# Kernel tuning notes

Measured on AMD Instinct MI355X. Metric: run time of the kernel, lower is better.

Reference implementation:

```python
import jax, jax.numpy as jnp
import numpy as np

B, T, C, H = 8, 1024, 768, 12  # GPT-2 small attention, block_size=1024

def setup_inputs() -> dict:
    key = jax.random.key(0)
    k0, k1, k2 = jax.random.split(key, 3)
    return {
        "x": jax.random.normal(k0, (1, B, T, C), jnp.float32) * 0.02,
        "w_attn": jax.random.normal(k1, (C, 3 * C), jnp.float32) * 0.02,
        "b_attn": jnp.zeros((3 * C,), jnp.float32),
        "w_proj": jax.random.normal(k2, (C, C), jnp.float32) * 0.02,
        "b_proj": jnp.zeros((C,), jnp.float32),
    }

def reference(x, w_attn, b_attn, w_proj, b_proj):
    _, b, t, c = x.shape
    d = c // H  # head dim
    xb = x[0]  # [B,T,C]
    qkv = xb @ w_attn + b_attn  # [B,T,3C]
    q, k, v = jnp.split(qkv, 3, axis=-1)
    def to_heads(u):
        return u.reshape(b, t, H, d).transpose(0, 2, 1, 3)  # [B,H,T,D]
    q, k, v = to_heads(q), to_heads(k), to_heads(v)
    scale = 1.0 / jnp.sqrt(jnp.asarray(d, q.dtype))
    att = jnp.einsum('bhqd,bhkd->bhqk', q, k) * scale  # [B,H,T,T]
    causal = jnp.tril(jnp.ones((t, t), bool))
    att = jnp.where(causal, att, -jnp.inf)
    att = jax.nn.softmax(att, axis=-1)
    y = jnp.einsum('bhqk,bhkd->bhqd', att, v)  # [B,H,T,D]
    y = y.transpose(0, 2, 1, 3).reshape(1, b, t, c)
    return y @ w_proj + b_proj
```

## Files before the change

kernel.cpp:

```cpp
#include <hip/hip_runtime.h>
#include <hip/hip_bf16.h>
#include <math.h>

#define Bq 8
#define Tq 1024
#define Cq 768
#define Hq 12
#define Dq 64
#define MROWS (Bq*Tq)
#define N_QKV (3*Cq)

typedef __bf16 bf16;
typedef bf16 bf16x8 __attribute__((ext_vector_type(8)));
typedef bf16 bf16x4 __attribute__((ext_vector_type(4)));
typedef float f32x4 __attribute__((ext_vector_type(4)));
typedef float f32x16 __attribute__((ext_vector_type(16)));
typedef unsigned int u32x4 __attribute__((ext_vector_type(4)));

#define MFMA16x16x32(a, b, c) __builtin_amdgcn_mfma_f32_16x16x32_bf16((a), (b), (c), 0, 0, 0)
#define MFMA32x32x16(a, b, c) __builtin_amdgcn_mfma_f32_32x32x16_bf16((a), (b), (c), 0, 0, 0)

__device__ __forceinline__ bf16x8& lds_v8(bf16* base, int row, int byteoff) {
    return *reinterpret_cast<bf16x8*>(
        reinterpret_cast<char*>(base) + row * 128 + (byteoff ^ ((row & 7) << 4)));
}

typedef __attribute__((address_space(3))) unsigned int lds_u32;
typedef const __attribute__((address_space(1))) unsigned int glb_u32;
__device__ __forceinline__ void gload16(const void* g, void* lds) {
    __builtin_amdgcn_global_load_lds((glb_u32*)(uintptr_t)g,
                                     (lds_u32*)(unsigned int)(uintptr_t)lds,
                                     16, 0, 0);
}

__device__ __forceinline__ unsigned cvtpk_bf16(float lo, float hi) {
    unsigned r;
    asm volatile("v_cvt_pk_bf16_f32 %0, %1, %2" : "=v"(r) : "v"(lo), "v"(hi));
    return r;
}

#define NA_CONV 3072
#define NB_WA   432
#define NB_WP   144
__global__ __launch_bounds__(256) void prep(const float* __restrict__ x,
                                            const float* __restrict__ wa,
                                            const float* __restrict__ wp,
                                            bf16* __restrict__ Ax,
                                            bf16* __restrict__ WaT,
                                            bf16* __restrict__ WpT) {
    __shared__ float tile[64][65];
    const int bid = blockIdx.x;
    if (bid < NA_CONV) {
        const int i = bid * 256 + threadIdx.x;
        const float4* p = reinterpret_cast<const float4*>(x) + (size_t)i * 2;
        float4 a = p[0], b = p[1];
        bf16x8 o;
        o[0] = (bf16)a.x; o[1] = (bf16)a.y; o[2] = (bf16)a.z; o[3] = (bf16)a.w;
        o[4] = (bf16)b.x; o[5] = (bf16)b.y; o[6] = (bf16)b.z; o[7] = (bf16)b.w;
        reinterpret_cast<bf16x8*>(Ax)[i] = o;
        return;
    }
    const float* src;
    bf16* dst;
    int C, tb, bxT;
    if (bid < NA_CONV + NB_WA) { tb = bid - NA_CONV; src = wa; dst = WaT; C = N_QKV; bxT = 36; }
    else                       { tb = bid - NA_CONV - NB_WA; src = wp; dst = WpT; C = Cq; bxT = 12; }
    const int R = Cq;
    const int bx = (tb % bxT) * 64, by = (tb / bxT) * 64;
    const int tx = threadIdx.x & 63, ty = threadIdx.x >> 6;
    #pragma unroll
    for (int i = 0; i < 64; i += 4)
        tile[ty + i][tx] = src[(size_t)(by + ty + i) * C + bx + tx];
    __syncthreads();
    #pragma unroll
    for (int i = 0; i < 64; i += 4)
        dst[(size_t)(bx + ty + i) * R + by + tx] = (bf16)tile[tx][ty + i];
}

__global__ __launch_bounds__(256) void gemm_qkv(const bf16* __restrict__ A,
                                                const bf16* __restrict__ Bt,
                                                const float* __restrict__ bias,
                                                bf16* __restrict__ Qo,
                                                bf16* __restrict__ Ko,
                                                bf16* __restrict__ Vto) {
    __shared__ bf16 As[2][128 * 64];
    __shared__ bf16 Bs[2][128 * 64];
    const int tid = threadIdx.x;
    const int w = tid >> 6, l = tid & 63;
    const int lane16 = l & 15, kg = l >> 4;
    const int wr = w >> 1, wc = w & 1;
    const int flat = blockIdx.x;
    const int nid = (flat & 7) * 144 + (flat >> 3);
    const int bn0 = (nid % 18) * 128, bm0 = (nid / 18) * 128;

    auto stage = [&](int k0, int buf) {
        #pragma unroll
        for (int j = 0; j < 4; ++j) {
            const int q8 = w * 4 + j;
            const int r  = q8 * 8 + (l >> 3);
            const int c16 = (l & 7) ^ (r & 7);
            gload16(A + (size_t)(bm0 + r) * Cq + k0 + c16 * 8, &As[buf][q8 * 512]);
            gload16(Bt + (size_t)(bn0 + r) * Cq + k0 + c16 * 8, &Bs[buf][q8 * 512]);
        }
    };

    f32x4 acc[4][4] = {};
    stage(0, 0);
    __syncthreads();
    for (int kt = 0; kt < 12; ++kt) {
        if (kt < 11) stage((kt + 1) * 64, (kt + 1) & 1);
        bf16* Ac = As[kt & 1];
        bf16* Bc = Bs[kt & 1];
        #pragma unroll
        for (int ks = 0; ks < 2; ++ks) {
            bf16x8 af[4], bfr[4];
            #pragma unroll
            for (int m = 0; m < 4; ++m)
                af[m] = lds_v8(Ac, wr * 64 + m * 16 + lane16, ks * 64 + kg * 16);
            #pragma unroll
            for (int n = 0; n < 4; ++n)
                bfr[n] = lds_v8(Bc, wc * 64 + n * 16 + lane16, ks * 64 + kg * 16);
            #pragma unroll
            for (int m = 0; m < 4; ++m)
                #pragma unroll
                for (int n = 0; n < 4; ++n)
                    acc[m][n] = MFMA16x16x32(af[m], bfr[n], acc[m][n]);
        }
        __syncthreads();
    }

    const int whichB = bn0 / Cq;
    char* Lt = (char*)&As[0][0];
    #pragma unroll
    for (int mi = 0; mi < 4; ++mi) {
        #pragma unroll
        for (int r = 0; r < 4; ++r) {
            const int m = wr * 64 + mi * 16 + kg * 4 + r;
            #pragma unroll
            for (int ni = 0; ni < 4; ++ni) {
                const int n = wc * 64 + ni * 16 + lane16;
                float v = acc[mi][ni][r] + bias[bn0 + n];
                if (whichB == 0) v *= 0.18033688011112042f;
                int a;
                if (whichB < 2) a = m * 256 + ((n * 2) ^ ((m & 7) << 4));
                else            a = n * 256 + ((m * 2) ^ ((n & 7) << 4));
                *reinterpret_cast<bf16*>(Lt + a) = (bf16)v;
            }
        }
    }
    __syncthreads();
    const int bb = bm0 >> 10, tt0 = bm0 & 1023;
    if (whichB < 2) {
        bf16* dst = whichB == 0 ? Qo : Ko;
        #pragma unroll
        for (int j = 0; j < 8; ++j) {
            const int c = j * 256 + tid;
            const int m = c >> 4, nc = c & 15;
            bf16x8 val = *reinterpret_cast<bf16x8*>(Lt + m * 256 + ((nc * 16) ^ ((m & 7) << 4)));
            const int gcol0 = bn0 + nc * 8;
            const int h = (gcol0 - whichB * Cq) >> 6;
            const int d0 = gcol0 & 63;
            *reinterpret_cast<bf16x8*>(dst + (((size_t)bb * Hq + h) * Tq + tt0 + m) * Dq + d0) = val;
        }
    } else {
        #pragma unroll
        for (int j = 0; j < 8; ++j) {
            const int c = j * 256 + tid;
            const int n = c >> 4, mc = c & 15;
            bf16x8 val = *reinterpret_cast<bf16x8*>(Lt + n * 256 + ((mc * 16) ^ ((n & 7) << 4)));
            const int gcol0 = bn0 + n;
            const int h = (gcol0 - 2 * Cq) >> 6;
            const int d = gcol0 & 63;
            *reinterpret_cast<bf16x8*>(Vto + (((size_t)bb * Hq + h) * Dq + d) * Tq + tt0 + mc * 8) = val;
        }
    }
}

__global__ __launch_bounds__(256) void attn_mfma(const bf16* __restrict__ Q,
                                                 const bf16* __restrict__ K,
                                                 const bf16* __restrict__ Vt,
                                                 bf16* __restrict__ Y) {
    const int tid = threadIdx.x;
    const int w = tid >> 6, l = tid & 63;
    const int l31 = l & 31, hi = l >> 5;
    const int g = blockIdx.x / 96;
    const int bh = blockIdx.x % 96;
    const int qs = 31 - (g * 4 + w);
    const int q0 = qs * 32;
    const int nt = (qs >> 1) + 1;
    const size_t hoff = (size_t)bh * Tq * Dq;

    bf16x8 qf[4];
    #pragma unroll
    for (int ds = 0; ds < 4; ++ds)
        qf[ds] = *reinterpret_cast<const bf16x8*>(
            Q + hoff + (size_t)(q0 + l31) * Dq + ds * 16 + hi * 8);

    f32x16 o[2] = {};
    float m_ = -INFINITY, l_ = 0.f;

    for (int t = 0; t < nt; ++t) {
        const bool diag = (t == nt - 1);
        const bool half = diag && !(qs & 1);
        const bf16* Kt  = K  + hoff + (size_t)(t * 64) * Dq;
        const bf16* Vtt = Vt + hoff + t * 64;

        bf16x8 kf0[4], kf1[4];
        #pragma unroll
        for (int ds = 0; ds < 4; ++ds)
            kf0[ds] = *reinterpret_cast<const bf16x8*>(
                Kt + (size_t)l31 * Dq + ds * 16 + hi * 8);
        if (!half) {
            #pragma unroll
            for (int ds = 0; ds < 4; ++ds)
                kf1[ds] = *reinterpret_cast<const bf16x8*>(
                    Kt + (size_t)(32 + l31) * Dq + ds * 16 + hi * 8);
        }
        bf16x8 vf[4][2];
        #pragma unroll
        for (int ks = 0; ks < 2; ++ks)
            #pragma unroll
            for (int dh = 0; dh < 2; ++dh)
                vf[ks][dh] = *reinterpret_cast<const bf16x8*>(
                    Vtt + (size_t)(dh * 32 + l31) * Tq + ks * 16 + hi * 8);
        if (!half) {
            #pragma unroll
            for (int ks = 2; ks < 4; ++ks)
                #pragma unroll
                for (int dh = 0; dh < 2; ++dh)
                    vf[ks][dh] = *reinterpret_cast<const bf16x8*>(
                        Vtt + (size_t)(dh * 32 + l31) * Tq + ks * 16 + hi * 8);
        }

        f32x16 s0 = {}, s1 = {};
        #pragma unroll
        for (int ds = 0; ds < 4; ++ds) s0 = MFMA32x32x16(kf0[ds], qf[ds], s0);
        if (!half) {
            #pragma unroll
            for (int ds = 0; ds < 4; ++ds) s1 = MFMA32x32x16(kf1[ds], qf[ds], s1);
        }
        if (diag) {
            #pragma unroll
            for (int reg = 0; reg < 16; ++reg) {
                const int kg_ = t * 64 + (reg & 3) + 8 * (reg >> 2) + 4 * hi;
                if (kg_ > q0 + l31) s0[reg] = -INFINITY;
                if (!half && kg_ + 32 > q0 + l31) s1[reg] = -INFINITY;
            }
        }
        float pmax = -INFINITY;
        #pragma unroll
        for (int reg = 0; reg < 16; ++reg) pmax = fmaxf(pmax, s0[reg]);
        if (!half) {
            #pragma unroll
            for (int reg = 0; reg < 16; ++reg) pmax = fmaxf(pmax, s1[reg]);
        }
        pmax = fmaxf(pmax, __shfl_xor(pmax, 32));
        if (!__all(pmax <= m_ + 8.f)) {
            const float mn = fmaxf(m_, pmax);
            const float alpha = exp2f(m_ - mn);
            m_ = mn;
            l_ *= alpha;
            o[0] *= alpha;
            o[1] *= alpha;
        }
        float lsum = 0.f;
        #pragma unroll
        for (int reg = 0; reg < 16; ++reg) {
            const float p = exp2f(s0[reg] - m_);
            s0[reg] = p;
            lsum += p;
        }
        if (!half) {
            #pragma unroll
            for (int reg = 0; reg < 16; ++reg) {
                const float p = exp2f(s1[reg] - m_);
                s1[reg] = p;
                lsum += p;
            }
        }
        l_ += lsum;

        bf16x8 pa[4];
        #pragma unroll
        for (int g2 = 0; g2 < 2; ++g2) {
            const int rb = g2 * 8;
            const unsigned u01 = cvtpk_bf16(s0[rb + 0], s0[rb + 1]);
            const unsigned u23 = cvtpk_bf16(s0[rb + 2], s0[rb + 3]);
            const unsigned u45 = cvtpk_bf16(s0[rb + 4], s0[rb + 5]);
            const unsigned u67 = cvtpk_bf16(s0[rb + 6], s0[rb + 7]);
            const unsigned x01 = __shfl_xor(u01, 32);
            const unsigned x23 = __shfl_xor(u23, 32);
            const unsigned x45 = __shfl_xor(u45, 32);
            const unsigned x67 = __shfl_xor(u67, 32);
            u32x4 wv;
            wv[0] = hi ? x45 : u01;
            wv[1] = hi ? x67 : u23;
            wv[2] = hi ? u45 : x01;
            wv[3] = hi ? u67 : x23;
            pa[g2] = __builtin_bit_cast(bf16x8, wv);
        }
        if (!half) {
            #pragma unroll
            for (int g2 = 0; g2 < 2; ++g2) {
                const int rb = g2 * 8;
                const unsigned u01 = cvtpk_bf16(s1[rb + 0], s1[rb + 1]);
                const unsigned u23 = cvtpk_bf16(s1[rb + 2], s1[rb + 3]);
                const unsigned u45 = cvtpk_bf16(s1[rb + 4], s1[rb + 5]);
                const unsigned u67 = cvtpk_bf16(s1[rb + 6], s1[rb + 7]);
                const unsigned x01 = __shfl_xor(u01, 32);
                const unsigned x23 = __shfl_xor(u23, 32);
                const unsigned x45 = __shfl_xor(u45, 32);
                const unsigned x67 = __shfl_xor(u67, 32);
                u32x4 wv;
                wv[0] = hi ? x45 : u01;
                wv[1] = hi ? x67 : u23;
                wv[2] = hi ? u45 : x01;
                wv[3] = hi ? u67 : x23;
                pa[2 + g2] = __builtin_bit_cast(bf16x8, wv);
            }
        }
        #pragma unroll
        for (int ks = 0; ks < 2; ++ks)
            #pragma unroll
            for (int dh = 0; dh < 2; ++dh)
                o[dh] = MFMA32x32x16(vf[ks][dh], pa[ks], o[dh]);
        if (!half) {
            #pragma unroll
            for (int ks = 2; ks < 4; ++ks)
                #pragma unroll
                for (int dh = 0; dh < 2; ++dh)
                    o[dh] = MFMA32x32x16(vf[ks][dh], pa[ks], o[dh]);
        }
    }

    const int bb = bh / Hq, h = bh - bb * Hq;
    const float ltot = l_ + __shfl_xor(l_, 32);
    const float inv = 1.f / ltot;
    bf16* yp = Y + ((size_t)bb * Tq + q0 + l31) * Cq + h * Dq;
    #pragma unroll
    for (int dh = 0; dh < 2; ++dh)
        #pragma unroll
        for (int rg = 0; rg < 4; ++rg) {
            const int d0 = 8 * rg + 4 * hi + 32 * dh;
            bf16x4 ov;
            #pragma unroll
            for (int j = 0; j < 4; ++j) ov[j] = (bf16)(o[dh][rg * 4 + j] * inv);
            *reinterpret_cast<bf16x4*>(yp + d0) = ov;
        }
}

__global__ __launch_bounds__(256) void gemm_proj(const bf16* __restrict__ A,
                                                 const bf16* __restrict__ Bt,
                                                 const float* __restrict__ bias,
                                                 float* __restrict__ out) {
    __shared__ bf16 As[2][128 * 64];
    __shared__ bf16 Bs[2][128 * 64];
    const int tid = threadIdx.x;
    const int w = tid >> 6, l = tid & 63;
    const int lane16 = l & 15, kg = l >> 4;
    const int wr = w >> 1, wc = w & 1;
    const int flat = blockIdx.x;
    const int nid = (flat & 7) * 48 + (flat >> 3);
    const int bn0 = (nid % 6) * 128, bm0 = (nid / 6) * 128;

    auto stage = [&](int k0, int buf) {
        #pragma unroll
        for (int j = 0; j < 4; ++j) {
            const int q8 = w * 4 + j;
            const int r  = q8 * 8 + (l >> 3);
            const int c16 = (l & 7) ^ (r & 7);
            gload16(A + (size_t)(bm0 + r) * Cq + k0 + c16 * 8, &As[buf][q8 * 512]);
            gload16(Bt + (size_t)(bn0 + r) * Cq + k0 + c16 * 8, &Bs[buf][q8 * 512]);
        }
    };

    f32x4 acc[4][4] = {};
    stage(0, 0);
    __syncthreads();
    for (int kt = 0; kt < 12; ++kt) {
        if (kt < 11) stage((kt + 1) * 64, (kt + 1) & 1);
        bf16* Ac = As[kt & 1];
        bf16* Bc = Bs[kt & 1];
        #pragma unroll
        for (int ks = 0; ks < 2; ++ks) {
            bf16x8 af[4], bfr[4];
            #pragma unroll
            for (int m = 0; m < 4; ++m)
                af[m] = lds_v8(Ac, wr * 64 + m * 16 + lane16, ks * 64 + kg * 16);
            #pragma unroll
            for (int n = 0; n < 4; ++n)
                bfr[n] = lds_v8(Bc, wc * 64 + n * 16 + lane16, ks * 64 + kg * 16);
            #pragma unroll
            for (int m = 0; m < 4; ++m)
                #pragma unroll
                for (int n = 0; n < 4; ++n)
                    acc[m][n] = MFMA16x16x32(af[m], bfr[n], acc[m][n]);
        }
        __syncthreads();
    }

    char* L32 = (char*)&As[0][0];
    #pragma unroll
    for (int half = 0; half < 2; ++half) {
        if (wc == half) {
            #pragma unroll
            for (int mi = 0; mi < 4; ++mi)
                #pragma unroll
                for (int r = 0; r < 4; ++r) {
                    const int m = wr * 64 + mi * 16 + kg * 4 + r;
                    #pragma unroll
                    for (int ni = 0; ni < 4; ++ni) {
                        const int nl = ni * 16 + lane16;
                        const float v = acc[mi][ni][r] + bias[bn0 + half * 64 + nl];
                        *reinterpret_cast<float*>(L32 + m * 256 + ((nl * 4) ^ ((m & 7) << 4))) = v;
                    }
                }
        }
        __syncthreads();
        #pragma unroll
        for (int j = 0; j < 8; ++j) {
            const int c = j * 256 + tid;
            const int m = c >> 4, nc = c & 15;
            float4 val = *reinterpret_cast<float4*>(L32 + m * 256 + ((nc * 16) ^ ((m & 7) << 4)));
            *reinterpret_cast<float4*>(out + (size_t)(bm0 + m) * Cq + bn0 + half * 64 + nc * 4) = val;
        }
        __syncthreads();
    }
}

extern "C" void kernel_launch(void* const* d_in, const int* in_sizes, int n_in,
                              void* d_out, int out_size, void* d_ws, size_t ws_size,
                              hipStream_t stream) {
    const float* x      = (const float*)d_in[0];
    const float* w_attn = (const float*)d_in[1];
    const float* b_attn = (const float*)d_in[2];
    const float* w_proj = (const float*)d_in[3];
    const float* b_proj = (const float*)d_in[4];
    float* out = (float*)d_out;

    char* ws = (char*)d_ws;
    bf16* Ax  = (bf16*)ws; ws += (size_t)MROWS * Cq * 2;
    bf16* WaT = (bf16*)ws; ws += (size_t)N_QKV * Cq * 2;
    bf16* WpT = (bf16*)ws; ws += (size_t)Cq * Cq * 2;
    bf16* Qw  = (bf16*)ws; ws += (size_t)MROWS * Cq * 2;
    bf16* Kw  = (bf16*)ws; ws += (size_t)MROWS * Cq * 2;
    bf16* Vtw = (bf16*)ws; ws += (size_t)MROWS * Cq * 2;
    bf16* Yw  = (bf16*)ws; ws += (size_t)MROWS * Cq * 2;

    prep<<<dim3(NA_CONV + NB_WA + NB_WP), 256, 0, stream>>>(x, w_attn, w_proj, Ax, WaT, WpT);
    gemm_qkv<<<dim3(1152), 256, 0, stream>>>(Ax, WaT, b_attn, Qw, Kw, Vtw);
    attn_mfma<<<dim3(768), 256, 0, stream>>>(Qw, Kw, Vtw, Yw);
    gemm_proj<<<dim3(384), 256, 0, stream>>>(Yw, WpT, b_proj, out);
}
```

Before: 125.0 us.

## Stage K/V tiles in double-buffered LDS shared across waves in attention

The attention kernel now loads each 64-key K and V^T tile once per block into a double-buffered, swizzled LDS buffer using async global-to-LDS loads, prefetching the next tile while computing the current one. Before, each wave read K/V directly from global memory. The block-to-(head, query-block) mapping is also rearranged so the four waves share a head and adjacent query slices, with XCD-aware ordering. This cuts redundant global traffic and overlaps loads with compute, but adds a __syncthreads per tile and makes waves with shorter causal ranges wait for the longest one.

```diff
diff --git a/kernel.cpp b/kernel.cpp
--- a/kernel.cpp
+++ b/kernel.cpp
@@ -180,14 +180,19 @@
                                                  const bf16* __restrict__ K,
                                                  const bf16* __restrict__ Vt,
                                                  bf16* __restrict__ Y) {
+    __shared__ bf16 Kl[2][64 * 64];
+    __shared__ bf16 Vl[2][64 * 64];
     const int tid = threadIdx.x;
     const int w = tid >> 6, l = tid & 63;
     const int l31 = l & 31, hi = l >> 5;
-    const int g = blockIdx.x / 96;
-    const int bh = blockIdx.x % 96;
-    const int qs = 31 - (g * 4 + w);
+    const int id = blockIdx.x;
+    const int xcd = id & 7, j = id >> 3;
+    const int bh = xcd * 12 + (j >> 3);
+    const int qb = 7 - (j & 7);
+    const int qs = qb * 4 + w;
     const int q0 = qs * 32;
     const int nt = (qs >> 1) + 1;
+    const int ntmax = 2 * qb + 2;
     const size_t hoff = (size_t)bh * Tq * Dq;
 
     bf16x8 qf[4];
@@ -199,114 +204,94 @@
     f32x16 o[2] = {};
     float m_ = -INFINITY, l_ = 0.f;
 
-    for (int t = 0; t < nt; ++t) {
-        const bool diag = (t == nt - 1);
-        const bool half = diag && !(qs & 1);
-        const bf16* Kt  = K  + hoff + (size_t)(t * 64) * Dq;
-        const bf16* Vtt = Vt + hoff + t * 64;
-
-        bf16x8 kf0[4], kf1[4];
-        #pragma unroll
-        for (int ds = 0; ds < 4; ++ds)
-            kf0[ds] = *reinterpret_cast<const bf16x8*>(
-                Kt + (size_t)l31 * Dq + ds * 16 + hi * 8);
-        if (!half) {
+    auto stage = [&](int t, int buf) {
+        #pragma unroll
+        for (int jj = 0; jj < 2; ++jj) {
+            const int q8 = w * 2 + jj;
+            const int r  = q8 * 8 + (l >> 3);
+            const int c16 = (l & 7) ^ (r & 7);
+            gload16(K + hoff + (size_t)(t * 64 + r) * Dq + c16 * 8, &Kl[buf][q8 * 512]);
+            gload16(Vt + hoff + (size_t)r * Tq + t * 64 + c16 * 8, &Vl[buf][q8 * 512]);
+        }
+    };
+
+    stage(0, 0);
+    __syncthreads();
+
+    for (int t = 0; t < ntmax; ++t) {
+        if (t + 1 < ntmax) stage(t + 1, (t + 1) & 1);
+        if (t < nt) {
+            bf16* Kc = Kl[t & 1];
+            bf16* Vc = Vl[t & 1];
+            const bool diag = (t == nt - 1);
+            const bool half = diag && !(qs & 1);
+
+            bf16x8 kf0[4], kf1[4];
             #pragma unroll
             for (int ds = 0; ds < 4; ++ds)
-                kf1[ds] = *reinterpret_cast<const bf16x8*>(
-                    Kt + (size_t)(32 + l31) * Dq + ds * 16 + hi * 8);
-        }
-        bf16x8 vf[4][2];
-        #pragma unroll
-        for (int ks = 0; ks < 2; ++ks)
-            #pragma unroll
-            for (int dh = 0; dh < 2; ++dh)
-                vf[ks][dh] = *reinterpret_cast<const bf16x8*>(
-                    Vtt + (size_t)(dh * 32 + l31) * Tq + ks * 16 + hi * 8);
-        if (!half) {
-            #pragma unroll
-            for (int ks = 2; ks < 4; ++ks)
-                #pragma unroll
-                for (int dh = 0; dh < 2; ++dh)
-                    vf[ks][dh] = *reinterpret_cast<const bf16x8*>(
-                        Vtt + (size_t)(dh * 32 + l31) * Tq + ks * 16 + hi * 8);
-        }
-
-        f32x16 s0 = {}, s1 = {};
-        #pragma unroll
-        for (int ds = 0; ds < 4; ++ds) s0 = MFMA32x32x16(kf0[ds], qf[ds], s0);
-        if (!half) {
-            #pragma unroll
-            for (int ds = 0; ds < 4; ++ds) s1 = MFMA32x32x16(kf1[ds], qf[ds], s1);
-        }
-        if (diag) {
+                kf0[ds] = lds_v8(Kc, l31, ds * 32 + hi * 16);
+            if (!half) {
+                #pragma unroll
+                for (int ds = 0; ds < 4; ++ds)
+                    kf1[ds] = lds_v8(Kc, 32 + l31, ds * 32 + hi * 16);
+            }
+
+            f32x16 s0 = {}, s1 = {};
+            #pragma unroll
+            for (int ds = 0; ds < 4; ++ds) s0 = MFMA32x32x16(kf0[ds], qf[ds], s0);
+            if (!half) {
+                #pragma unroll
+                for (int ds = 0; ds < 4; ++ds) s1 = MFMA32x32x16(kf1[ds], qf[ds], s1);
+            }
+            if (diag) {
+                #pragma unroll
+                for (int reg = 0; reg < 16; ++reg) {
+                    const int kg_ = t * 64 + (reg & 3) + 8 * (reg >> 2) + 4 * hi;
+                    if (kg_ > q0 + l31) s0[reg] = -INFINITY;
+                    if (!half && kg_ + 32 > q0 + l31) s1[reg] = -INFINITY;
+                }
+            }
+            float pmax = -INFINITY;
+            #pragma unroll
+            for (int reg = 0; reg < 16; ++reg) pmax = fmaxf(pmax, s0[reg]);
+            if (!half) {
+                #pragma unroll
+                for (int reg = 0; reg < 16; ++reg) pmax = fmaxf(pmax, s1[reg]);
+            }
+            pmax = fmaxf(pmax, __shfl_xor(pmax, 32));
+            if (!__all(pmax <= m_ + 8.f)) {
+                const float mn = fmaxf(m_, pmax);
+                const float alpha = exp2f(m_ - mn);
+                m_ = mn;
+                l_ *= alpha;
+                o[0] *= alpha;
+                o[1] *= alpha;
+            }
+            float lsum = 0.f;
             #pragma unroll
             for (int reg = 0; reg < 16; ++reg) {
-                const int kg_ = t * 64 + (reg & 3) + 8 * (reg >> 2) + 4 * hi;
-                if (kg_ > q0 + l31) s0[reg] = -INFINITY;
-                if (!half && kg_ + 32 > q0 + l31) s1[reg] = -INFINITY;
-            }
-        }
-        float pmax = -INFINITY;
-        #pragma unroll
-        for (int reg = 0; reg < 16; ++reg) pmax = fmaxf(pmax, s0[reg]);
-        if (!half) {
-            #pragma unroll
-            for (int reg = 0; reg < 16; ++reg) pmax = fmaxf(pmax, s1[reg]);
-        }
-        pmax = fmaxf(pmax, __shfl_xor(pmax, 32));
-        if (!__all(pmax <= m_ + 8.f)) {
-            const float mn = fmaxf(m_, pmax);
-            const float alpha = exp2f(m_ - mn);
-            m_ = mn;
-            l_ *= alpha;
-            o[0] *= alpha;
-            o[1] *= alpha;
-        }
-        float lsum = 0.f;
-        #pragma unroll
-        for (int reg = 0; reg < 16; ++reg) {
-            const float p = exp2f(s0[reg] - m_);
-            s0[reg] = p;
-            lsum += p;
-        }
-        if (!half) {
-            #pragma unroll
-            for (int reg = 0; reg < 16; ++reg) {
-                const float p = exp2f(s1[reg] - m_);
-                s1[reg] = p;
+                const float p = exp2f(s0[reg] - m_);
+                s0[reg] = p;
                 lsum += p;
             }
-        }
-        l_ += lsum;
-
-        bf16x8 pa[4];
-        #pragma unroll
-        for (int g2 = 0; g2 < 2; ++g2) {
-            const int rb = g2 * 8;
-            const unsigned u01 = cvtpk_bf16(s0[rb + 0], s0[rb + 1]);
-            const unsigned u23 = cvtpk_bf16(s0[rb + 2], s0[rb + 3]);
-            const unsigned u45 = cvtpk_bf16(s0[rb + 4], s0[rb + 5]);
-            const unsigned u67 = cvtpk_bf16(s0[rb + 6], s0[rb + 7]);
-            const unsigned x01 = __shfl_xor(u01, 32);
-            const unsigned x23 = __shfl_xor(u23, 32);
-            const unsigned x45 = __shfl_xor(u45, 32);
-            const unsigned x67 = __shfl_xor(u67, 32);
-            u32x4 wv;
-            wv[0] = hi ? x45 : u01;
-            wv[1] = hi ? x67 : u23;
-            wv[2] = hi ? u45 : x01;
-            wv[3] = hi ? u67 : x23;
-            pa[g2] = __builtin_bit_cast(bf16x8, wv);
-        }
-        if (!half) {
+            if (!half) {
+                #pragma unroll
+                for (int reg = 0; reg < 16; ++reg) {
+                    const float p = exp2f(s1[reg] - m_);
+                    s1[reg] = p;
+                    lsum += p;
+                }
+            }
+            l_ += lsum;
+
+            bf16x8 pa[4];
             #pragma unroll
             for (int g2 = 0; g2 < 2; ++g2) {
                 const int rb = g2 * 8;
-                const unsigned u01 = cvtpk_bf16(s1[rb + 0], s1[rb + 1]);
-                const unsigned u23 = cvtpk_bf16(s1[rb + 2], s1[rb + 3]);
-                const unsigned u45 = cvtpk_bf16(s1[rb + 4], s1[rb + 5]);
-                const unsigned u67 = cvtpk_bf16(s1[rb + 6], s1[rb + 7]);
+                const unsigned u01 = cvtpk_bf16(s0[rb + 0], s0[rb + 1]);
+                const unsigned u23 = cvtpk_bf16(s0[rb + 2], s0[rb + 3]);
+                const unsigned u45 = cvtpk_bf16(s0[rb + 4], s0[rb + 5]);
+                const unsigned u67 = cvtpk_bf16(s0[rb + 6], s0[rb + 7]);
                 const unsigned x01 = __shfl_xor(u01, 32);
                 const unsigned x23 = __shfl_xor(u23, 32);
                 const unsigned x45 = __shfl_xor(u45, 32);
@@ -316,21 +301,46 @@
                 wv[1] = hi ? x67 : u23;
                 wv[2] = hi ? u45 : x01;
                 wv[3] = hi ? u67 : x23;
-                pa[2 + g2] = __builtin_bit_cast(bf16x8, wv);
-            }
-        }
-        #pragma unroll
-        for (int ks = 0; ks < 2; ++ks)
-            #pragma unroll
-            for (int dh = 0; dh < 2; ++dh)
-                o[dh] = MFMA32x32x16(vf[ks][dh], pa[ks], o[dh]);
-        if (!half) {
-            #pragma unroll
-            for (int ks = 2; ks < 4; ++ks)
-                #pragma unroll
-                for (int dh = 0; dh < 2; ++dh)
-                    o[dh] = MFMA32x32x16(vf[ks][dh], pa[ks], o[dh]);
-        }
+                pa[g2] = __builtin_bit_cast(bf16x8, wv);
+            }
+            if (!half) {
+                #pragma unroll
+                for (int g2 = 0; g2 < 2; ++g2) {
+                    const int rb = g2 * 8;
+                    const unsigned u01 = cvtpk_bf16(s1[rb + 0], s1[rb + 1]);
+                    const unsigned u23 = cvtpk_bf16(s1[rb + 2], s1[rb + 3]);
+                    const unsigned u45 = cvtpk_bf16(s1[rb + 4], s1[rb + 5]);
+                    const unsigned u67 = cvtpk_bf16(s1[rb + 6], s1[rb + 7]);
+                    const unsigned x01 = __shfl_xor(u01, 32);
+                    const unsigned x23 = __shfl_xor(u23, 32);
+                    const unsigned x45 = __shfl_xor(u45, 32);
+                    const unsigned x67 = __shfl_xor(u67, 32);
+                    u32x4 wv;
+                    wv[0] = hi ? x45 : u01;
+                    wv[1] = hi ? x67 : u23;
+                    wv[2] = hi ? u45 : x01;
+                    wv[3] = hi ? u67 : x23;
+                    pa[2 + g2] = __builtin_bit_cast(bf16x8, wv);
+                }
+            }
+            #pragma unroll
+            for (int ks = 0; ks < 2; ++ks)
+                #pragma unroll
+                for (int dh = 0; dh < 2; ++dh) {
+                    bf16x8 vfr = lds_v8(Vc, dh * 32 + l31, ks * 32 + hi * 16);
+                    o[dh] = MFMA32x32x16(vfr, pa[ks], o[dh]);
+                }
+            if (!half) {
+                #pragma unroll
+                for (int ks = 2; ks < 4; ++ks)
+                    #pragma unroll
+                    for (int dh = 0; dh < 2; ++dh) {
+                        bf16x8 vfr = lds_v8(Vc, dh * 32 + l31, ks * 32 + hi * 16);
+                        o[dh] = MFMA32x32x16(vfr, pa[ks], o[dh]);
+                    }
+            }
+        }
+        __syncthreads();
     }
 
     const int bb = bh / Hq, h = bh - bb * Hq;
@@ -344,7 +354,7 @@
             const int d0 = 8 * rg + 4 * hi + 32 * dh;
             bf16x4 ov;
             #pragma unroll
-            for (int j = 0; j < 4; ++j) ov[j] = (bf16)(o[dh][rg * 4 + j] * inv);
+            for (int jj = 0; jj < 4; ++jj) ov[jj] = (bf16)(o[dh][rg * 4 + jj] * inv);
             *reinterpret_cast<bf16x4*>(yp + d0) = ov;
         }
 }
```

After: 135.1 us. 8.1% more time.

## Repack K and V into 8-element chunked layouts and use permlane32 swap in attention

Applied to the files above, without the earlier changes.

The QKV GEMM epilogue now writes K and V in chunked layouts where each lane's 16-byte fragment sits next to its neighbours, so the attention kernel's K and V loads become contiguous across lanes instead of strided by head dim or sequence length. The P-fragment rearrangement swaps shuffle-plus-select for v_permlane32_swap. The max and sum reductions are split into four independent accumulators to shorten dependency chains. The conditional lazy rescale is removed, so the output is now rescaled on every tile, which adds some VALU work.

```diff
diff --git a/kernel.cpp b/kernel.cpp
--- a/kernel.cpp
+++ b/kernel.cpp
@@ -37,6 +37,10 @@
     unsigned r;
     asm volatile("v_cvt_pk_bf16_f32 %0, %1, %2" : "=v"(r) : "v"(lo), "v"(hi));
     return r;
+}
+
+__device__ __forceinline__ void permlane32_swap(unsigned& a, unsigned& b) {
+    asm("v_permlane32_swap_b32 %0, %1" : "+v"(a), "+v"(b));
 }
 
 #define NA_CONV 3072
@@ -81,8 +85,8 @@
                                                 const bf16* __restrict__ Bt,
                                                 const float* __restrict__ bias,
                                                 bf16* __restrict__ Qo,
-                                                bf16* __restrict__ Ko,
-                                                bf16* __restrict__ Vto) {
+                                                bf16* __restrict__ K8,
+                                                bf16* __restrict__ V8) {
     __shared__ bf16 As[2][128 * 64];
     __shared__ bf16 Bs[2][128 * 64];
     const int tid = threadIdx.x;
@@ -150,35 +154,47 @@
     }
     __syncthreads();
     const int bb = bm0 >> 10, tt0 = bm0 & 1023;
-    if (whichB < 2) {
-        bf16* dst = whichB == 0 ? Qo : Ko;
+    if (whichB == 0) {
         #pragma unroll
         for (int j = 0; j < 8; ++j) {
             const int c = j * 256 + tid;
             const int m = c >> 4, nc = c & 15;
             bf16x8 val = *reinterpret_cast<bf16x8*>(Lt + m * 256 + ((nc * 16) ^ ((m & 7) << 4)));
             const int gcol0 = bn0 + nc * 8;
-            const int h = (gcol0 - whichB * Cq) >> 6;
+            const int h = gcol0 >> 6;
             const int d0 = gcol0 & 63;
-            *reinterpret_cast<bf16x8*>(dst + (((size_t)bb * Hq + h) * Tq + tt0 + m) * Dq + d0) = val;
-        }
-    } else {
+            *reinterpret_cast<bf16x8*>(Qo + (((size_t)bb * Hq + h) * Tq + tt0 + m) * Dq + d0) = val;
+        }
+    } else if (whichB == 1) {
         #pragma unroll
         for (int j = 0; j < 8; ++j) {
             const int c = j * 256 + tid;
-            const int n = c >> 4, mc = c & 15;
+            const int m = c & 127, nc = c >> 7;
+            bf16x8 val = *reinterpret_cast<bf16x8*>(Lt + m * 256 + ((nc * 16) ^ ((m & 7) << 4)));
+            const int hn = bn0 + nc * 8 - Cq;
+            const int h = hn >> 6, d8 = (hn >> 3) & 7;
+            *reinterpret_cast<bf16x8*>(
+                K8 + ((((size_t)bb * Hq + h) * 8 + d8) * Tq + tt0 + m) * 8) = val;
+        }
+    } else {
+        #pragma unroll
+        for (int j = 0; j < 8; ++j) {
+            const int c = j * 256 + tid;
+            const int d6 = c & 63, rest = c >> 6;
+            const int hh = rest & 1, mc = rest >> 1;
+            const int n = hh * 64 + d6;
             bf16x8 val = *reinterpret_cast<bf16x8*>(Lt + n * 256 + ((mc * 16) ^ ((n & 7) << 4)));
-            const int gcol0 = bn0 + n;
-            const int h = (gcol0 - 2 * Cq) >> 6;
-            const int d = gcol0 & 63;
-            *reinterpret_cast<bf16x8*>(Vto + (((size_t)bb * Hq + h) * Dq + d) * Tq + tt0 + mc * 8) = val;
+            const int hn = bn0 + n - 2 * Cq;
+            const int h = hn >> 6, d = hn & 63;
+            *reinterpret_cast<bf16x8*>(
+                V8 + ((((size_t)bb * Hq + h) * 128 + (tt0 >> 3) + mc) * Dq + d) * 8) = val;
         }
     }
 }
 
 __global__ __launch_bounds__(256) void attn_mfma(const bf16* __restrict__ Q,
-                                                 const bf16* __restrict__ K,
-                                                 const bf16* __restrict__ Vt,
+                                                 const bf16* __restrict__ K8,
+                                                 const bf16* __restrict__ V8,
                                                  bf16* __restrict__ Y) {
     const int tid = threadIdx.x;
     const int w = tid >> 6, l = tid & 63;
@@ -189,12 +205,14 @@
     const int q0 = qs * 32;
     const int nt = (qs >> 1) + 1;
     const size_t hoff = (size_t)bh * Tq * Dq;
+    const size_t base8 = (size_t)bh * (Tq * Dq);
+    const int q0g = q0 + l31;
 
     bf16x8 qf[4];
     #pragma unroll
     for (int ds = 0; ds < 4; ++ds)
         qf[ds] = *reinterpret_cast<const bf16x8*>(
-            Q + hoff + (size_t)(q0 + l31) * Dq + ds * 16 + hi * 8);
+            Q + hoff + (size_t)q0g * Dq + ds * 16 + hi * 8);
 
     f32x16 o[2] = {};
     float m_ = -INFINITY, l_ = 0.f;
@@ -202,19 +220,16 @@
     for (int t = 0; t < nt; ++t) {
         const bool diag = (t == nt - 1);
         const bool half = diag && !(qs & 1);
-        const bf16* Kt  = K  + hoff + (size_t)(t * 64) * Dq;
-        const bf16* Vtt = Vt + hoff + t * 64;
-
-        bf16x8 kf0[4], kf1[4];
+        bf16x8 kf[2][4];
         #pragma unroll
         for (int ds = 0; ds < 4; ++ds)
-            kf0[ds] = *reinterpret_cast<const bf16x8*>(
-                Kt + (size_t)l31 * Dq + ds * 16 + hi * 8);
+            kf[0][ds] = *reinterpret_cast<const bf16x8*>(
+                K8 + base8 + ((size_t)(ds * 2 + hi) * Tq + t * 64 + l31) * 8);
         if (!half) {
             #pragma unroll
             for (int ds = 0; ds < 4; ++ds)
-                kf1[ds] = *reinterpret_cast<const bf16x8*>(
-                    Kt + (size_t)(32 + l31) * Dq + ds * 16 + hi * 8);
+                kf[1][ds] = *reinterpret_cast<const bf16x8*>(
+                    K8 + base8 + ((size_t)(ds * 2 + hi) * Tq + t * 64 + 32 + l31) * 8);
         }
         bf16x8 vf[4][2];
         #pragma unroll
@@ -222,100 +237,108 @@
             #pragma unroll
             for (int dh = 0; dh < 2; ++dh)
                 vf[ks][dh] = *reinterpret_cast<const bf16x8*>(
-                    Vtt + (size_t)(dh * 32 + l31) * Tq + ks * 16 + hi * 8);
+                    V8 + base8 + ((size_t)(t * 8 + ks * 2 + hi) * Dq + dh * 32 + l31) * 8);
         if (!half) {
             #pragma unroll
             for (int ks = 2; ks < 4; ++ks)
                 #pragma unroll
                 for (int dh = 0; dh < 2; ++dh)
                     vf[ks][dh] = *reinterpret_cast<const bf16x8*>(
-                        Vtt + (size_t)(dh * 32 + l31) * Tq + ks * 16 + hi * 8);
-        }
-
-        f32x16 s0 = {}, s1 = {};
-        #pragma unroll
-        for (int ds = 0; ds < 4; ++ds) s0 = MFMA32x32x16(kf0[ds], qf[ds], s0);
-        if (!half) {
-            #pragma unroll
-            for (int ds = 0; ds < 4; ++ds) s1 = MFMA32x32x16(kf1[ds], qf[ds], s1);
+                        V8 + base8 + ((size_t)(t * 8 + ks * 2 + hi) * Dq + dh * 32 + l31) * 8);
+        }
+
+        f32x16 s[2] = {};
+        #pragma unroll
+        for (int ds = 0; ds < 4; ++ds) s[0] = MFMA32x32x16(kf[0][ds], qf[ds], s[0]);
+        if (!half) {
+            #pragma unroll
+            for (int ds = 0; ds < 4; ++ds) s[1] = MFMA32x32x16(kf[1][ds], qf[ds], s[1]);
         }
         if (diag) {
             #pragma unroll
             for (int reg = 0; reg < 16; ++reg) {
                 const int kg_ = t * 64 + (reg & 3) + 8 * (reg >> 2) + 4 * hi;
-                if (kg_ > q0 + l31) s0[reg] = -INFINITY;
-                if (!half && kg_ + 32 > q0 + l31) s1[reg] = -INFINITY;
+                if (kg_ > q0g) s[0][reg] = -INFINITY;
+                if (!half && kg_ + 32 > q0g) s[1][reg] = -INFINITY;
             }
         }
-        float pmax = -INFINITY;
-        #pragma unroll
-        for (int reg = 0; reg < 16; ++reg) pmax = fmaxf(pmax, s0[reg]);
-        if (!half) {
-            #pragma unroll
-            for (int reg = 0; reg < 16; ++reg) pmax = fmaxf(pmax, s1[reg]);
-        }
+        float pm0 = -INFINITY, pm1 = -INFINITY, pm2 = -INFINITY, pm3 = -INFINITY;
+        #pragma unroll
+        for (int reg = 0; reg < 16; reg += 4) {
+            pm0 = fmaxf(pm0, s[0][reg + 0]);
+            pm1 = fmaxf(pm1, s[0][reg + 1]);
+            pm2 = fmaxf(pm2, s[0][reg + 2]);
+            pm3 = fmaxf(pm3, s[0][reg + 3]);
+        }
+        if (!half) {
+            #pragma unroll
+            for (int reg = 0; reg < 16; reg += 4) {
+                pm0 = fmaxf(pm0, s[1][reg + 0]);
+                pm1 = fmaxf(pm1, s[1][reg + 1]);
+                pm2 = fmaxf(pm2, s[1][reg + 2]);
+                pm3 = fmaxf(pm3, s[1][reg + 3]);
+            }
+        }
+        float pmax = fmaxf(fmaxf(pm0, pm1), fmaxf(pm2, pm3));
         pmax = fmaxf(pmax, __shfl_xor(pmax, 32));
-        if (!__all(pmax <= m_ + 8.f)) {
-            const float mn = fmaxf(m_, pmax);
-            const float alpha = exp2f(m_ - mn);
-            m_ = mn;
-            l_ *= alpha;
-            o[0] *= alpha;
-            o[1] *= alpha;
-        }
-        float lsum = 0.f;
-        #pragma unroll
-        for (int reg = 0; reg < 16; ++reg) {
-            const float p = exp2f(s0[reg] - m_);
-            s0[reg] = p;
-            lsum += p;
-        }
-        if (!half) {
-            #pragma unroll
-            for (int reg = 0; reg < 16; ++reg) {
-                const float p = exp2f(s1[reg] - m_);
-                s1[reg] = p;
-                lsum += p;
+        const float mn = fmaxf(m_, pmax);
+        const float alpha = exp2f(m_ - mn);
+        m_ = mn;
+        l_ *= alpha;
+        o[0] *= alpha;
+        o[1] *= alpha;
+        float ls0 = 0.f, ls1 = 0.f, ls2 = 0.f, ls3 = 0.f;
+        #pragma unroll
+        for (int reg = 0; reg < 16; reg += 4) {
+            const float p0 = exp2f(s[0][reg + 0] - mn);
+            const float p1 = exp2f(s[0][reg + 1] - mn);
+            const float p2 = exp2f(s[0][reg + 2] - mn);
+            const float p3 = exp2f(s[0][reg + 3] - mn);
+            s[0][reg + 0] = p0; ls0 += p0;
+            s[0][reg + 1] = p1; ls1 += p1;
+            s[0][reg + 2] = p2; ls2 += p2;
+            s[0][reg + 3] = p3; ls3 += p3;
+        }
+        if (!half) {
+            #pragma unroll
+            for (int reg = 0; reg < 16; reg += 4) {
+                const float p0 = exp2f(s[1][reg + 0] - mn);
+                const float p1 = exp2f(s[1][reg + 1] - mn);
+                const float p2 = exp2f(s[1][reg + 2] - mn);
+                const float p3 = exp2f(s[1][reg + 3] - mn);
+                s[1][reg + 0] = p0; ls0 += p0;
+                s[1][reg + 1] = p1; ls1 += p1;
+                s[1][reg + 2] = p2; ls2 += p2;
+                s[1][reg + 3] = p3; ls3 += p3;
             }
         }
-        l_ += lsum;
-
+        l_ += (ls0 + ls1) + (ls2 + ls3);
         bf16x8 pa[4];
         #pragma unroll
         for (int g2 = 0; g2 < 2; ++g2) {
             const int rb = g2 * 8;
-            const unsigned u01 = cvtpk_bf16(s0[rb + 0], s0[rb + 1]);
-            const unsigned u23 = cvtpk_bf16(s0[rb + 2], s0[rb + 3]);
-            const unsigned u45 = cvtpk_bf16(s0[rb + 4], s0[rb + 5]);
-            const unsigned u67 = cvtpk_bf16(s0[rb + 6], s0[rb + 7]);
-            const unsigned x01 = __shfl_xor(u01, 32);
-            const unsigned x23 = __shfl_xor(u23, 32);
-            const unsigned x45 = __shfl_xor(u45, 32);
-            const unsigned x67 = __shfl_xor(u67, 32);
+            unsigned u01 = cvtpk_bf16(s[0][rb + 0], s[0][rb + 1]);
+            unsigned u23 = cvtpk_bf16(s[0][rb + 2], s[0][rb + 3]);
+            unsigned u45 = cvtpk_bf16(s[0][rb + 4], s[0][rb + 5]);
+            unsigned u67 = cvtpk_bf16(s[0][rb + 6], s[0][rb + 7]);
+            permlane32_swap(u01, u45);
+            permlane32_swap(u23, u67);
             u32x4 wv;
-            wv[0] = hi ? x45 : u01;
-            wv[1] = hi ? x67 : u23;
-            wv[2] = hi ? u45 : x01;
-            wv[3] = hi ? u67 : x23;
+            wv[0] = u01; wv[1] = u23; wv[2] = u45; wv[3] = u67;
             pa[g2] = __builtin_bit_cast(bf16x8, wv);
         }
         if (!half) {
             #pragma unroll
             for (int g2 = 0; g2 < 2; ++g2) {
                 const int rb = g2 * 8;
-                const unsigned u01 = cvtpk_bf16(s1[rb + 0], s1[rb + 1]);
-                const unsigned u23 = cvtpk_bf16(s1[rb + 2], s1[rb + 3]);
-                const unsigned u45 = cvtpk_bf16(s1[rb + 4], s1[rb + 5]);
-                const unsigned u67 = cvtpk_bf16(s1[rb + 6], s1[rb + 7]);
-                const unsigned x01 = __shfl_xor(u01, 32);
-                const unsigned x23 = __shfl_xor(u23, 32);
-                const unsigned x45 = __shfl_xor(u45, 32);
-                const unsigned x67 = __shfl_xor(u67, 32);
+                unsigned u01 = cvtpk_bf16(s[1][rb + 0], s[1][rb + 1]);
+                unsigned u23 = cvtpk_bf16(s[1][rb + 2], s[1][rb + 3]);
+                unsigned u45 = cvtpk_bf16(s[1][rb + 4], s[1][rb + 5]);
+                unsigned u67 = cvtpk_bf16(s[1][rb + 6], s[1][rb + 7]);
+                permlane32_swap(u01, u45);
+                permlane32_swap(u23, u67);
                 u32x4 wv;
-                wv[0] = hi ? x45 : u01;
-                wv[1] = hi ? x67 : u23;
-                wv[2] = hi ? u45 : x01;
-                wv[3] = hi ? u67 : x23;
+                wv[0] = u01; wv[1] = u23; wv[2] = u45; wv[3] = u67;
                 pa[2 + g2] = __builtin_bit_cast(bf16x8, wv);
             }
         }
@@ -336,7 +359,7 @@
     const int bb = bh / Hq, h = bh - bb * Hq;
     const float ltot = l_ + __shfl_xor(l_, 32);
     const float inv = 1.f / ltot;
-    bf16* yp = Y + ((size_t)bb * Tq + q0 + l31) * Cq + h * Dq;
+    bf16* yp = Y + ((size_t)bb * Tq + q0g) * Cq + h * Dq;
     #pragma unroll
     for (int dh = 0; dh < 2; ++dh)
         #pragma unroll
@@ -443,12 +466,12 @@
     bf16* WaT = (bf16*)ws; ws += (size_t)N_QKV * Cq * 2;
     bf16* WpT = (bf16*)ws; ws += (size_t)Cq * Cq * 2;
     bf16* Qw  = (bf16*)ws; ws += (size_t)MROWS * Cq * 2;
-    bf16* Kw  = (bf16*)ws; ws += (size_t)MROWS * Cq * 2;
-    bf16* Vtw = (bf16*)ws; ws += (size_t)MROWS * Cq * 2;
+    bf16* K8w = (bf16*)ws; ws += (size_t)MROWS * Cq * 2;
+    bf16* V8w = (bf16*)ws; ws += (size_t)MROWS * Cq * 2;
     bf16* Yw  = (bf16*)ws; ws += (size_t)MROWS * Cq * 2;
 
     prep<<<dim3(NA_CONV + NB_WA + NB_WP), 256, 0, stream>>>(x, w_attn, w_proj, Ax, WaT, WpT);
-    gemm_qkv<<<dim3(1152), 256, 0, stream>>>(Ax, WaT, b_attn, Qw, Kw, Vtw);
-    attn_mfma<<<dim3(768), 256, 0, stream>>>(Qw, Kw, Vtw, Yw);
+    gemm_qkv<<<dim3(1152), 256, 0, stream>>>(Ax, WaT, b_attn, Qw, K8w, V8w);
+    attn_mfma<<<dim3(768), 256, 0, stream>>>(Qw, K8w, V8w, Yw);
     gemm_proj<<<dim3(384), 256, 0, stream>>>(Yw, WpT, b_proj, out);
 }
```

Measured after the change: 108.2 us. 1.16x faster.
